# Kernel tuning notes

Hardware: AMD Instinct MI355X
Metric: run time of the kernel (lower is better)

The kernel has to match this reference:

```python
import jax, jax.numpy as jnp
import numpy as np

B, D, H, K = 32768, 64, 512, 8
P = 3 * K - 1            # widths(K) + heights(K) + interior derivatives(K-1)
BOUND = 4.0
MIN_BIN = 1e-3           # min bin width/height fraction
MIN_DERIV = 1e-3


def setup_inputs() -> dict:
    key = jax.random.key(0)
    k0, k1, k2, k3 = jax.random.split(key, 4)
    x = jax.random.normal(k0, (B, D), jnp.float32) * 2.0
    W1 = jax.random.normal(k1, (H, D), jnp.float32) / np.sqrt(D)
    b1 = jnp.zeros((H,), jnp.float32)
    W2 = jax.random.normal(k2, (D * P, H), jnp.float32) / np.sqrt(H)
    b2 = jax.random.normal(k3, (D * P,), jnp.float32) * 0.01
    m_in = np.arange(1, D + 1)                      # input degrees 1..D
    m_hid = (np.arange(H) % (D - 1)) + 1            # hidden degrees 1..D-1
    M1 = jnp.asarray((m_hid[:, None] >= m_in[None, :]).astype(np.float32))   # [H, D]
    m_out = (np.arange(D * P) // P) + 1             # output degree = dim index + 1
    M2 = jnp.asarray((m_out[:, None] > m_hid[None, :]).astype(np.float32))   # [D*P, H]
    return {"x": x, "W1": W1, "b1": b1, "W2": W2, "b2": b2, "M1": M1, "M2": M2}


def _rqs(x, w_un, h_un, d_un):
    """Monotonic rational-quadratic spline (elementwise over [B, D]).
    w_un, h_un: [B, D, K] unnormalized widths/heights; d_un: [B, D, K-1].
    Returns (y [B, D], logabsdet [B, D])."""
    f32 = x.dtype
    w = jax.nn.softmax(w_un, axis=-1)
    hh = jax.nn.softmax(h_un, axis=-1)
    w = MIN_BIN + (1.0 - MIN_BIN * K) * w
    hh = MIN_BIN + (1.0 - MIN_BIN * K) * hh
    edge_lo = jnp.full(w.shape[:-1] + (1,), -BOUND, f32)
    edge_hi = jnp.full(w.shape[:-1] + (1,), BOUND, f32)
    # knot positions [B, D, K+1] with exact endpoints at +-BOUND
    xk = jnp.concatenate([edge_lo, -BOUND + 2.0 * BOUND * jnp.cumsum(w, -1)[..., :-1], edge_hi], -1)
    yk = jnp.concatenate([edge_lo, -BOUND + 2.0 * BOUND * jnp.cumsum(hh, -1)[..., :-1], edge_hi], -1)
    widths = xk[..., 1:] - xk[..., :-1]
    heights = yk[..., 1:] - yk[..., :-1]
    ones = jnp.ones(w.shape[:-1] + (1,), f32)
    # boundary derivatives fixed to 1 (identity outside the box)
    d = jnp.concatenate([ones, MIN_DERIV + jax.nn.softplus(d_un), ones], -1)  # [B, D, K+1]

    inside = (x >= -BOUND) & (x <= BOUND)
    xc = jnp.clip(x, -BOUND, BOUND)
    # bucketize: index of containing bin
    idx = jnp.clip(jnp.sum((xc[..., None] >= xk).astype(jnp.int32), -1) - 1, 0, K - 1)

    def g(a, off=0):
        return jnp.take_along_axis(a, idx[..., None] + off, axis=-1)[..., 0]

    x_k, y_k = g(xk), g(yk)
    w_k, h_k = g(widths), g(heights)
    d_k, d_k1 = g(d), g(d, 1)
    s = h_k / w_k
    theta = (xc - x_k) / w_k
    t1m = theta * (1.0 - theta)
    num = h_k * (s * theta * theta + d_k * t1m)
    den = s + (d_k1 + d_k - 2.0 * s) * t1m
    y_in = y_k + num / den
    dnum = s * s * (d_k1 * theta * theta + 2.0 * s * t1m + d_k * (1.0 - theta) ** 2)
    ld_in = jnp.log(dnum) - 2.0 * jnp.log(den)
    y = jnp.where(inside, y_in, x)
    ld = jnp.where(inside, ld_in, 0.0)
    return y, ld


def _forward(x, W1, b1, W2, b2, M1, M2):
    hmid = jax.nn.relu(x @ (W1 * M1).T + b1)          # [B, H]
    params = (hmid @ (W2 * M2).T + b2).reshape(x.shape[0], D, P)
    w_un = params[..., :K]
    h_un = params[..., K:2 * K]
    d_un = params[..., 2 * K:]
    z, ld = _rqs(x, w_un, h_un, d_un)
    return z, jnp.sum(ld, axis=-1)                    # logDet per example


def reference(x, W1, b1, W2, b2, M1, M2):
    return _forward(x, W1, b1, W2, b2, M1, M2)
```

## Files before the change

kernel.cpp:

```cpp
#include <hip/hip_runtime.h>
#include <math.h>

#define NB    32768
#define DDIM  64
#define HDIM  512
#define PDIM  23
#define KBINS 8
#define BM    32
#define NCOLS (DDIM * PDIM)
#define CHUNK 368
#define PSTRIDE 372
#define NTILES 92

#define RQ_BOUND  4.0f
#define RQ_MINBIN 0.001f
#define RQ_MINDER 0.001f

typedef __attribute__((ext_vector_type(8))) _Float16 half8;
typedef __attribute__((ext_vector_type(4))) float f32x4;
typedef unsigned short ushort_t;

__global__ __launch_bounds__(256) void prep_frag(const float* __restrict__ W1,
                                                 const float* __restrict__ W2,
                                                 _Float16* __restrict__ W1g,
                                                 _Float16* __restrict__ W2g) {
    const int gid = blockIdx.x * 256 + threadIdx.x;
    const int NW1 = 32 * 2 * 64;
    if (gid < NW1) {
        const int lane = gid & 63;
        const int tk   = gid >> 6;
        const int kt   = tk & 1, ht = tk >> 1;
        const int h = ht * 16 + (lane & 15);
        const int k = kt * 32 + (lane >> 4) * 8;
        const float* src = W1 + h * DDIM + k;
        const int hm63 = h % 63;
        half8 v;
        #pragma unroll
        for (int e = 0; e < 8; ++e)
            v[e] = (_Float16)(((k + e) <= hm63) ? src[e] : 0.0f);
        *(half8*)(W1g + (size_t)gid * 8) = v;
    } else {
        const int g2 = gid - NW1;
        if (g2 < NTILES * 16 * 64) {
            const int lane = g2 & 63;
            const int tk   = g2 >> 6;
            const int kt   = tk & 15, T = tk >> 4;
            const int col  = T * 16 + (lane & 15);
            const int k    = kt * 32 + (lane >> 4) * 8;
            const float* src = W2 + (size_t)col * HDIM + k;
            const int d = col / PDIM;
            half8 v;
            #pragma unroll
            for (int e = 0; e < 8; ++e)
                v[e] = (_Float16)((d > ((k + e) % 63)) ? src[e] : 0.0f);
            *(half8*)(W2g + (size_t)g2 * 8) = v;
        }
    }
}

__device__ __forceinline__ float fexp(float v)  { return __expf(v); }
__device__ __forceinline__ float flog(float v)  { return __logf(v); }
__device__ __forceinline__ float fdiv(float a, float b) { return __fdividef(a, b); }

__device__ __forceinline__ void rqs_eval(const float* prm, float xorig,
                                         float& yo, float& ldo) {
    const float xc = fminf(fmaxf(xorig, -RQ_BOUND), RQ_BOUND);
    const bool inside = (xorig >= -RQ_BOUND) && (xorig <= RQ_BOUND);

    float xk[KBINS + 1], yk[KBINS + 1], dd[KBINS + 1];
    {
        float m = prm[0];
        #pragma unroll
        for (int i = 1; i < KBINS; ++i) m = fmaxf(m, prm[i]);
        float e[KBINS]; float s = 0.0f;
        #pragma unroll
        for (int i = 0; i < KBINS; ++i) { e[i] = fexp(prm[i] - m); s += e[i]; }
        const float inv = fdiv(1.0f, s);
        float c = 0.0f;
        xk[0] = -RQ_BOUND;
        #pragma unroll
        for (int i = 0; i < KBINS; ++i) {
            float w = RQ_MINBIN + (1.0f - RQ_MINBIN * KBINS) * (e[i] * inv);
            c += w;
            xk[i + 1] = -RQ_BOUND + 2.0f * RQ_BOUND * c;
        }
        xk[KBINS] = RQ_BOUND;
    }
    {
        float m = prm[8];
        #pragma unroll
        for (int i = 1; i < KBINS; ++i) m = fmaxf(m, prm[8 + i]);
        float e[KBINS]; float s = 0.0f;
        #pragma unroll
        for (int i = 0; i < KBINS; ++i) { e[i] = fexp(prm[8 + i] - m); s += e[i]; }
        const float inv = fdiv(1.0f, s);
        float c = 0.0f;
        yk[0] = -RQ_BOUND;
        #pragma unroll
        for (int i = 0; i < KBINS; ++i) {
            float h = RQ_MINBIN + (1.0f - RQ_MINBIN * KBINS) * (e[i] * inv);
            c += h;
            yk[i + 1] = -RQ_BOUND + 2.0f * RQ_BOUND * c;
        }
        yk[KBINS] = RQ_BOUND;
    }
    dd[0] = 1.0f;
    #pragma unroll
    for (int i = 0; i < KBINS - 1; ++i) {
        const float v = prm[16 + i];
        const float e = fexp(-fabsf(v));
        dd[i + 1] = RQ_MINDER + flog(1.0f + e) + fmaxf(v, 0.0f);
    }
    dd[KBINS] = 1.0f;

    int idx = 0;
    #pragma unroll
    for (int i = 1; i < KBINS; ++i) idx += (xc >= xk[i]) ? 1 : 0;

    float x_k = xk[0], x_k1 = xk[1];
    float y_k = yk[0], y_k1 = yk[1];
    float d_k = dd[0], d_k1 = dd[1];
    #pragma unroll
    for (int i = 1; i < KBINS; ++i) {
        const bool mm = (idx == i);
        x_k  = mm ? xk[i]     : x_k;
        x_k1 = mm ? xk[i + 1] : x_k1;
        y_k  = mm ? yk[i]     : y_k;
        y_k1 = mm ? yk[i + 1] : y_k1;
        d_k  = mm ? dd[i]     : d_k;
        d_k1 = mm ? dd[i + 1] : d_k1;
    }

    const float w_k = x_k1 - x_k;
    const float h_k = y_k1 - y_k;
    const float rw  = fdiv(1.0f, w_k);
    const float s   = h_k * rw;
    const float th  = (xc - x_k) * rw;
    const float omt = 1.0f - th;
    const float t1m = th * omt;
    const float num = h_k * (s * th * th + d_k * t1m);
    const float den = s + (d_k1 + d_k - 2.0f * s) * t1m;
    const float yin = y_k + fdiv(num, den);
    const float dnum = s * s * (d_k1 * th * th + 2.0f * s * t1m + d_k * omt * omt);
    const float ldin = flog(dnum) - 2.0f * flog(den);

    yo  = inside ? yin : xorig;
    ldo = inside ? ldin : 0.0f;
}

__global__ __launch_bounds__(512, 4) void fused_flow(
    const float* __restrict__ x,  const float* __restrict__ b1,
    const float* __restrict__ b2, const _Float16* __restrict__ W1g,
    const _Float16* __restrict__ W2g,
    float* __restrict__ z_out, float* __restrict__ ld_out)
{
    __shared__ __align__(16) ushort_t hm[BM * 512];
    __shared__ __align__(16) float pstage[BM * PSTRIDE];

    const int t    = threadIdx.x;
    const int row0 = blockIdx.x * BM;
    const int wv   = t >> 6;
    const int lane = t & 63;
    const int l15  = lane & 15;
    const int lg   = lane >> 4;

    char* hmB = (char*)hm;

    {
        f32x4 acc1[4][2];
        #pragma unroll
        for (int j = 0; j < 4; ++j)
            #pragma unroll
            for (int m = 0; m < 2; ++m) acc1[j][m] = (f32x4){0.f, 0.f, 0.f, 0.f};

        #pragma unroll
        for (int kt = 0; kt < 2; ++kt) {
            half8 a[2];
            #pragma unroll
            for (int m = 0; m < 2; ++m) {
                const float* xr = x + (size_t)(row0 + m * 16 + l15) * DDIM + kt * 32 + lg * 8;
                const float4 xa = *(const float4*)(xr);
                const float4 xb = *(const float4*)(xr + 4);
                a[m][0] = (_Float16)xa.x; a[m][1] = (_Float16)xa.y;
                a[m][2] = (_Float16)xa.z; a[m][3] = (_Float16)xa.w;
                a[m][4] = (_Float16)xb.x; a[m][5] = (_Float16)xb.y;
                a[m][6] = (_Float16)xb.z; a[m][7] = (_Float16)xb.w;
            }
            #pragma unroll
            for (int j = 0; j < 4; ++j) {
                const half8 b = *(const half8*)(W1g + (size_t)(wv * 4 + j) * 1024 + kt * 512 + lane * 8);
                #pragma unroll
                for (int m = 0; m < 2; ++m)
                    acc1[j][m] = __builtin_amdgcn_mfma_f32_16x16x32_f16(a[m], b, acc1[j][m], 0, 0, 0);
            }
        }
        #pragma unroll
        for (int j = 0; j < 4; ++j) {
            const int h = (wv * 4 + j) * 16 + l15;
            const float bias = b1[h];
            #pragma unroll
            for (int m = 0; m < 2; ++m) {
                #pragma unroll
                for (int q = 0; q < 4; ++q) {
                    const int r = m * 16 + lg * 4 + q;
                    const _Float16 hv = (_Float16)fmaxf(acc1[j][m][q] + bias, 0.0f);
                    *(ushort_t*)(hmB + r * 1024 + ((h * 2) ^ ((r & 7) << 4))) =
                        __builtin_bit_cast(ushort_t, hv);
                }
            }
        }
    }
    __syncthreads();

    float ldacc = 0.0f;
    const int srow = t >> 4;
    const int sd   = t & 15;
    const int tbase = wv * 3;

    const _Float16* w2base[3];
    #pragma unroll
    for (int i = 0; i < 3; ++i) {
        const int tile = (tbase + i < 23) ? (tbase + i) : 22;
        w2base[i] = W2g + (size_t)tile * 8192 + lane * 8;
    }

    for (int c = 0; c < 4; ++c) {
        f32x4 acc[3][2];
        #pragma unroll
        for (int i = 0; i < 3; ++i)
            #pragma unroll
            for (int m = 0; m < 2; ++m) acc[i][m] = (f32x4){0.f, 0.f, 0.f, 0.f};

        const size_t coff = (size_t)c * (23 * 8192);

        #pragma unroll 4
        for (int kt = 0; kt < 16; ++kt) {
            half8 ah[2];
            #pragma unroll
            for (int m = 0; m < 2; ++m) {
                const int r  = m * 16 + l15;
                const int kb = (kt * 32 + lg * 8) * 2;
                ah[m] = *(const half8*)(hmB + r * 1024 + (kb ^ ((r & 7) << 4)));
            }
            half8 bfr[3];
            #pragma unroll
            for (int i = 0; i < 3; ++i)
                bfr[i] = *(const half8*)(w2base[i] + coff + kt * 512);
            #pragma unroll
            for (int i = 0; i < 3; ++i)
                #pragma unroll
                for (int m = 0; m < 2; ++m)
                    acc[i][m] = __builtin_amdgcn_mfma_f32_16x16x32_f16(ah[m], bfr[i], acc[i][m], 0, 0, 0);
        }

        __syncthreads();

        #pragma unroll
        for (int i = 0; i < 3; ++i) {
            if (tbase + i < 23) {
                const int lcol = (tbase + i) * 16 + l15;
                #pragma unroll
                for (int m = 0; m < 2; ++m)
                    #pragma unroll
                    for (int q = 0; q < 4; ++q)
                        pstage[(m * 16 + lg * 4 + q) * PSTRIDE + lcol] = acc[i][m][q];
            }
        }
        __syncthreads();

        {
            const int d = c * 16 + sd;
            float prm[PDIM];
            #pragma unroll
            for (int p = 0; p < PDIM; ++p)
                prm[p] = pstage[srow * PSTRIDE + sd * PDIM + p] + b2[d * PDIM + p];
            const float xv = x[(size_t)(row0 + srow) * DDIM + d];
            float yv, lv;
            rqs_eval(prm, xv, yv, lv);
            z_out[(size_t)(row0 + srow) * DDIM + d] = yv;
            ldacc += lv;
        }
    }

    ldacc += __shfl_xor(ldacc, 1, 64);
    ldacc += __shfl_xor(ldacc, 2, 64);
    ldacc += __shfl_xor(ldacc, 4, 64);
    ldacc += __shfl_xor(ldacc, 8, 64);
    if (sd == 0) ld_out[row0 + srow] = ldacc;
}

extern "C" void kernel_launch(void* const* d_in, const int* in_sizes, int n_in,
                              void* d_out, int out_size, void* d_ws, size_t ws_size,
                              hipStream_t stream) {
    (void)in_sizes; (void)n_in; (void)out_size; (void)ws_size;
    const float* x  = (const float*)d_in[0];
    const float* W1 = (const float*)d_in[1];
    const float* b1 = (const float*)d_in[2];
    const float* W2 = (const float*)d_in[3];
    const float* b2 = (const float*)d_in[4];

    _Float16* W1g = (_Float16*)d_ws;
    _Float16* W2g = W1g + HDIM * DDIM;
    float* z  = (float*)d_out;
    float* ld = z + (size_t)NB * DDIM;

    const int n_groups = 32 * 2 * 64 + NTILES * 16 * 64;
    prep_frag<<<(n_groups + 255) / 256, 256, 0, stream>>>(W1, W2, W1g, W2g);
    fused_flow<<<NB / BM, 512, 0, stream>>>(x, b1, b2, W1g, W2g, z, ld);
}
```

Baseline: 93.57 us.

## Prefetch next chunk's W2 fragments and simplify spline math

New measurement: 92.47 us. No clear change (-1.2%).

```diff
diff --git a/kernel.cpp b/kernel.cpp
--- a/kernel.cpp
+++ b/kernel.cpp
@@ -66,51 +66,41 @@
                                          float& yo, float& ldo) {
     const float xc = fminf(fmaxf(xorig, -RQ_BOUND), RQ_BOUND);
     const bool inside = (xorig >= -RQ_BOUND) && (xorig <= RQ_BOUND);
+    const float CNORM = 1.0f - RQ_MINBIN * KBINS;
 
     float xk[KBINS + 1], yk[KBINS + 1], dd[KBINS + 1];
     {
-        float m = prm[0];
-        #pragma unroll
-        for (int i = 1; i < KBINS; ++i) m = fmaxf(m, prm[i]);
         float e[KBINS]; float s = 0.0f;
         #pragma unroll
-        for (int i = 0; i < KBINS; ++i) { e[i] = fexp(prm[i] - m); s += e[i]; }
-        const float inv = fdiv(1.0f, s);
+        for (int i = 0; i < KBINS; ++i) { e[i] = fexp(prm[i]); s += e[i]; }
+        const float cinv = CNORM * fdiv(1.0f, s);
         float c = 0.0f;
         xk[0] = -RQ_BOUND;
         #pragma unroll
         for (int i = 0; i < KBINS; ++i) {
-            float w = RQ_MINBIN + (1.0f - RQ_MINBIN * KBINS) * (e[i] * inv);
-            c += w;
-            xk[i + 1] = -RQ_BOUND + 2.0f * RQ_BOUND * c;
+            c += fmaf(e[i], cinv, RQ_MINBIN);
+            xk[i + 1] = fmaf(c, 2.0f * RQ_BOUND, -RQ_BOUND);
         }
         xk[KBINS] = RQ_BOUND;
     }
     {
-        float m = prm[8];
-        #pragma unroll
-        for (int i = 1; i < KBINS; ++i) m = fmaxf(m, prm[8 + i]);
         float e[KBINS]; float s = 0.0f;
         #pragma unroll
-        for (int i = 0; i < KBINS; ++i) { e[i] = fexp(prm[8 + i] - m); s += e[i]; }
-        const float inv = fdiv(1.0f, s);
+        for (int i = 0; i < KBINS; ++i) { e[i] = fexp(prm[8 + i]); s += e[i]; }
+        const float cinv = CNORM * fdiv(1.0f, s);
         float c = 0.0f;
         yk[0] = -RQ_BOUND;
         #pragma unroll
         for (int i = 0; i < KBINS; ++i) {
-            float h = RQ_MINBIN + (1.0f - RQ_MINBIN * KBINS) * (e[i] * inv);
-            c += h;
-            yk[i + 1] = -RQ_BOUND + 2.0f * RQ_BOUND * c;
+            c += fmaf(e[i], cinv, RQ_MINBIN);
+            yk[i + 1] = fmaf(c, 2.0f * RQ_BOUND, -RQ_BOUND);
         }
         yk[KBINS] = RQ_BOUND;
     }
     dd[0] = 1.0f;
     #pragma unroll
-    for (int i = 0; i < KBINS - 1; ++i) {
-        const float v = prm[16 + i];
-        const float e = fexp(-fabsf(v));
-        dd[i + 1] = RQ_MINDER + flog(1.0f + e) + fmaxf(v, 0.0f);
-    }
+    for (int i = 0; i < KBINS - 1; ++i)
+        dd[i + 1] = RQ_MINDER + flog(1.0f + fexp(prm[16 + i]));
     dd[KBINS] = 1.0f;
 
     int idx = 0;
@@ -142,7 +132,7 @@
     const float den = s + (d_k1 + d_k - 2.0f * s) * t1m;
     const float yin = y_k + fdiv(num, den);
     const float dnum = s * s * (d_k1 * th * th + 2.0f * s * t1m + d_k * omt * omt);
-    const float ldin = flog(dnum) - 2.0f * flog(den);
+    const float ldin = flog(fdiv(dnum, den * den));
 
     yo  = inside ? yin : xorig;
     ldo = inside ? ldin : 0.0f;
@@ -224,6 +214,13 @@
         w2base[i] = W2g + (size_t)tile * 8192 + lane * 8;
     }
 
+    half8 pfb0[3], pfb1[3];
+    #pragma unroll
+    for (int i = 0; i < 3; ++i) {
+        pfb0[i] = *(const half8*)(w2base[i]);
+        pfb1[i] = *(const half8*)(w2base[i] + 512);
+    }
+
     for (int c = 0; c < 4; ++c) {
         f32x4 acc[3][2];
         #pragma unroll
@@ -233,8 +230,8 @@
 
         const size_t coff = (size_t)c * (23 * 8192);
 
-        #pragma unroll 4
-        for (int kt = 0; kt < 16; ++kt) {
+        #pragma unroll
+        for (int kt = 0; kt < 2; ++kt) {
             half8 ah[2];
             #pragma unroll
             for (int m = 0; m < 2; ++m) {
@@ -242,6 +239,24 @@
                 const int kb = (kt * 32 + lg * 8) * 2;
                 ah[m] = *(const half8*)(hmB + r * 1024 + (kb ^ ((r & 7) << 4)));
             }
+            #pragma unroll
+            for (int i = 0; i < 3; ++i) {
+                const half8 bf = (kt == 0) ? pfb0[i] : pfb1[i];
+                #pragma unroll
+                for (int m = 0; m < 2; ++m)
+                    acc[i][m] = __builtin_amdgcn_mfma_f32_16x16x32_f16(ah[m], bf, acc[i][m], 0, 0, 0);
+            }
+        }
+
+        #pragma unroll 2
+        for (int kt = 2; kt < 16; ++kt) {
+            half8 ah[2];
+            #pragma unroll
+            for (int m = 0; m < 2; ++m) {
+                const int r  = m * 16 + l15;
+                const int kb = (kt * 32 + lg * 8) * 2;
+                ah[m] = *(const half8*)(hmB + r * 1024 + (kb ^ ((r & 7) << 4)));
+            }
             half8 bfr[3];
             #pragma unroll
             for (int i = 0; i < 3; ++i)
@@ -267,6 +282,15 @@
             }
         }
         __syncthreads();
+
+        {
+            const size_t ncoff = (size_t)(c < 3 ? c + 1 : 3) * (23 * 8192);
+            #pragma unroll
+            for (int i = 0; i < 3; ++i) {
+                pfb0[i] = *(const half8*)(w2base[i] + ncoff);
+                pfb1[i] = *(const half8*)(w2base[i] + ncoff + 512);
+            }
+        }
 
         {
             const int d = c * 16 + sd;
```

## Warp-specialize GEMM producers and spline consumers with double-buffered param staging

Applied to the files above, without the earlier changes.

After: 95.46 us. 2.0% more time.

```diff
diff --git a/kernel.cpp b/kernel.cpp
--- a/kernel.cpp
+++ b/kernel.cpp
@@ -8,9 +8,11 @@
 #define KBINS 8
 #define BM    32
 #define NCOLS (DDIM * PDIM)
-#define CHUNK 368
-#define PSTRIDE 372
-#define NTILES 92
+#define CH2   184
+#define NCH   8
+#define TPC   12
+#define PSTR2 185
+#define PBUFH (BM * PSTR2)
 
 #define RQ_BOUND  4.0f
 #define RQ_MINBIN 0.001f
@@ -41,11 +43,14 @@
         *(half8*)(W1g + (size_t)gid * 8) = v;
     } else {
         const int g2 = gid - NW1;
-        if (g2 < NTILES * 16 * 64) {
+        if (g2 < 96 * 16 * 64) {
             const int lane = g2 & 63;
             const int tk   = g2 >> 6;
-            const int kt   = tk & 15, T = tk >> 4;
-            const int col  = T * 16 + (lane & 15);
+            const int kt   = tk & 15, tt = tk >> 4;
+            const int c    = tt / TPC;
+            const int i    = tt - c * TPC;
+            const int colbase = c * CH2 + (i < 11 ? i * 16 : 168);
+            const int col  = colbase + (lane & 15);
             const int k    = kt * 32 + (lane >> 4) * 8;
             const float* src = W2 + (size_t)col * HDIM + k;
             const int d = col / PDIM;
@@ -66,51 +71,41 @@
                                          float& yo, float& ldo) {
     const float xc = fminf(fmaxf(xorig, -RQ_BOUND), RQ_BOUND);
     const bool inside = (xorig >= -RQ_BOUND) && (xorig <= RQ_BOUND);
+    const float CNORM = 1.0f - RQ_MINBIN * KBINS;
 
     float xk[KBINS + 1], yk[KBINS + 1], dd[KBINS + 1];
     {
-        float m = prm[0];
-        #pragma unroll
-        for (int i = 1; i < KBINS; ++i) m = fmaxf(m, prm[i]);
         float e[KBINS]; float s = 0.0f;
         #pragma unroll
-        for (int i = 0; i < KBINS; ++i) { e[i] = fexp(prm[i] - m); s += e[i]; }
-        const float inv = fdiv(1.0f, s);
+        for (int i = 0; i < KBINS; ++i) { e[i] = fexp(prm[i]); s += e[i]; }
+        const float cinv = CNORM * fdiv(1.0f, s);
         float c = 0.0f;
         xk[0] = -RQ_BOUND;
         #pragma unroll
         for (int i = 0; i < KBINS; ++i) {
-            float w = RQ_MINBIN + (1.0f - RQ_MINBIN * KBINS) * (e[i] * inv);
-            c += w;
-            xk[i + 1] = -RQ_BOUND + 2.0f * RQ_BOUND * c;
+            c += fmaf(e[i], cinv, RQ_MINBIN);
+            xk[i + 1] = fmaf(c, 2.0f * RQ_BOUND, -RQ_BOUND);
         }
         xk[KBINS] = RQ_BOUND;
     }
     {
-        float m = prm[8];
-        #pragma unroll
-        for (int i = 1; i < KBINS; ++i) m = fmaxf(m, prm[8 + i]);
         float e[KBINS]; float s = 0.0f;
         #pragma unroll
-        for (int i = 0; i < KBINS; ++i) { e[i] = fexp(prm[8 + i] - m); s += e[i]; }
-        const float inv = fdiv(1.0f, s);
+        for (int i = 0; i < KBINS; ++i) { e[i] = fexp(prm[8 + i]); s += e[i]; }
+        const float cinv = CNORM * fdiv(1.0f, s);
         float c = 0.0f;
         yk[0] = -RQ_BOUND;
         #pragma unroll
         for (int i = 0; i < KBINS; ++i) {
-            float h = RQ_MINBIN + (1.0f - RQ_MINBIN * KBINS) * (e[i] * inv);
-            c += h;
-            yk[i + 1] = -RQ_BOUND + 2.0f * RQ_BOUND * c;
+            c += fmaf(e[i], cinv, RQ_MINBIN);
+            yk[i + 1] = fmaf(c, 2.0f * RQ_BOUND, -RQ_BOUND);
         }
         yk[KBINS] = RQ_BOUND;
     }
     dd[0] = 1.0f;
     #pragma unroll
-    for (int i = 0; i < KBINS - 1; ++i) {
-        const float v = prm[16 + i];
-        const float e = fexp(-fabsf(v));
-        dd[i + 1] = RQ_MINDER + flog(1.0f + e) + fmaxf(v, 0.0f);
-    }
+    for (int i = 0; i < KBINS - 1; ++i)
+        dd[i + 1] = RQ_MINDER + flog(1.0f + fexp(prm[16 + i]));
     dd[KBINS] = 1.0f;
 
     int idx = 0;
@@ -142,7 +137,7 @@
     const float den = s + (d_k1 + d_k - 2.0f * s) * t1m;
     const float yin = y_k + fdiv(num, den);
     const float dnum = s * s * (d_k1 * th * th + 2.0f * s * t1m + d_k * omt * omt);
-    const float ldin = flog(dnum) - 2.0f * flog(den);
+    const float ldin = flog(fdiv(dnum, den * den));
 
     yo  = inside ? yin : xorig;
     ldo = inside ? ldin : 0.0f;
@@ -155,7 +150,7 @@
     float* __restrict__ z_out, float* __restrict__ ld_out)
 {
     __shared__ __align__(16) ushort_t hm[BM * 512];
-    __shared__ __align__(16) float pstage[BM * PSTRIDE];
+    __shared__ __align__(16) float pbuf[2 * PBUFH];
 
     const int t    = threadIdx.x;
     const int row0 = blockIdx.x * BM;
@@ -212,27 +207,29 @@
     }
     __syncthreads();
 
+    const bool producer = (wv < 6);
+    const int  tloc = t - 384;
+    const int  srow = tloc & 31;
+    const int  dq   = tloc >> 5;
+
+    const _Float16* w2base[2];
+    #pragma unroll
+    for (int i = 0; i < 2; ++i) {
+        const int j = (2 * wv + i < TPC) ? (2 * wv + i) : (TPC - 1);
+        w2base[i] = W2g + (size_t)j * 8192 + lane * 8;
+    }
+
     float ldacc = 0.0f;
-    const int srow = t >> 4;
-    const int sd   = t & 15;
-    const int tbase = wv * 3;
-
-    const _Float16* w2base[3];
-    #pragma unroll
-    for (int i = 0; i < 3; ++i) {
-        const int tile = (tbase + i < 23) ? (tbase + i) : 22;
-        w2base[i] = W2g + (size_t)tile * 8192 + lane * 8;
-    }
-
-    for (int c = 0; c < 4; ++c) {
-        f32x4 acc[3][2];
-        #pragma unroll
-        for (int i = 0; i < 3; ++i)
+    float z0a, z0b, z1a, z1b, z2a, z2b, z3a, z3b;
+    float z4a, z4b, z5a, z5b, z6a, z6b, z7a, z7b;
+
+    auto PROD = [&](int C) {
+        f32x4 acc[2][2];
+        #pragma unroll
+        for (int i = 0; i < 2; ++i)
             #pragma unroll
             for (int m = 0; m < 2; ++m) acc[i][m] = (f32x4){0.f, 0.f, 0.f, 0.f};
-
-        const size_t coff = (size_t)c * (23 * 8192);
-
+        const size_t coff = (size_t)C * (TPC * 8192);
         #pragma unroll 4
         for (int kt = 0; kt < 16; ++kt) {
             half8 ah[2];
@@ -242,51 +239,87 @@
                 const int kb = (kt * 32 + lg * 8) * 2;
                 ah[m] = *(const half8*)(hmB + r * 1024 + (kb ^ ((r & 7) << 4)));
             }
-            half8 bfr[3];
-            #pragma unroll
-            for (int i = 0; i < 3; ++i)
+            half8 bfr[2];
+            #pragma unroll
+            for (int i = 0; i < 2; ++i)
                 bfr[i] = *(const half8*)(w2base[i] + coff + kt * 512);
             #pragma unroll
-            for (int i = 0; i < 3; ++i)
+            for (int i = 0; i < 2; ++i)
                 #pragma unroll
                 for (int m = 0; m < 2; ++m)
                     acc[i][m] = __builtin_amdgcn_mfma_f32_16x16x32_f16(ah[m], bfr[i], acc[i][m], 0, 0, 0);
         }
-
-        __syncthreads();
-
-        #pragma unroll
-        for (int i = 0; i < 3; ++i) {
-            if (tbase + i < 23) {
-                const int lcol = (tbase + i) * 16 + l15;
+        float* pb = pbuf + (C & 1) * PBUFH;
+        #pragma unroll
+        for (int i = 0; i < 2; ++i) {
+            const int j = 2 * wv + i;
+            const int lcol = (j < 11 ? j * 16 : 168) + l15;
+            if (j < 11 || l15 >= 8) {
+                const float bb = b2[C * CH2 + lcol];
                 #pragma unroll
                 for (int m = 0; m < 2; ++m)
                     #pragma unroll
                     for (int q = 0; q < 4; ++q)
-                        pstage[(m * 16 + lg * 4 + q) * PSTRIDE + lcol] = acc[i][m][q];
-            }
-        }
-        __syncthreads();
-
-        {
-            const int d = c * 16 + sd;
-            float prm[PDIM];
-            #pragma unroll
-            for (int p = 0; p < PDIM; ++p)
-                prm[p] = pstage[srow * PSTRIDE + sd * PDIM + p] + b2[d * PDIM + p];
-            const float xv = x[(size_t)(row0 + srow) * DDIM + d];
-            float yv, lv;
-            rqs_eval(prm, xv, yv, lv);
-            z_out[(size_t)(row0 + srow) * DDIM + d] = yv;
-            ldacc += lv;
-        }
-    }
-
-    ldacc += __shfl_xor(ldacc, 1, 64);
-    ldacc += __shfl_xor(ldacc, 2, 64);
-    ldacc += __shfl_xor(ldacc, 4, 64);
-    ldacc += __shfl_xor(ldacc, 8, 64);
-    if (sd == 0) ld_out[row0 + srow] = ldacc;
+                        pb[(m * 16 + lg * 4 + q) * PSTR2 + lcol] = acc[i][m][q] + bb;
+            }
+        }
+    };
+
+    auto EVAL = [&](int sc, int dloc, float& zdst) {
+        const float* pb = pbuf + (sc & 1) * PBUFH + srow * PSTR2 + dloc * PDIM;
+        float prm[PDIM];
+        #pragma unroll
+        for (int p = 0; p < PDIM; ++p) prm[p] = pb[p];
+        const int d = sc * 8 + dloc;
+        const float xv = x[(size_t)(row0 + srow) * DDIM + d];
+        float yv, lv;
+        rqs_eval(prm, xv, yv, lv);
+        zdst = yv;
+        ldacc += lv;
+    };
+
+    #define STEP(C, ZA, ZB)                                             \
+        __syncthreads();                                                \
+        if (producer) { PROD(C); }                                      \
+        else { EVAL(C - 1, dq, ZA); EVAL(C - 1, dq + 4, ZB); }
+
+    __syncthreads();
+    if (producer) PROD(0);
+    STEP(1, z0a, z0b)
+    STEP(2, z1a, z1b)
+    STEP(3, z2a, z2b)
+    STEP(4, z3a, z3b)
+    STEP(5, z4a, z4b)
+    STEP(6, z5a, z5b)
+    STEP(7, z6a, z6b)
+    __syncthreads();
+    if (!producer) { EVAL(7, dq, z7a); EVAL(7, dq + 4, z7b); }
+    #undef STEP
+
+    if (!producer) {
+        float* zls = pbuf;
+        #define ZSC(SC, ZA, ZB)                         \
+            zls[srow * 65 + SC * 8 + dq]     = ZA;      \
+            zls[srow * 65 + SC * 8 + dq + 4] = ZB;
+        ZSC(0, z0a, z0b) ZSC(1, z1a, z1b) ZSC(2, z2a, z2b) ZSC(3, z3a, z3b)
+        ZSC(4, z4a, z4b) ZSC(5, z5a, z5b) ZSC(6, z6a, z6b) ZSC(7, z7a, z7b)
+        #undef ZSC
+        ldacc += __shfl_xor(ldacc, 32, 64);
+        if (lane < 32) zls[2080 + (wv - 6) * 32 + srow] = ldacc;
+    }
+    __syncthreads();
+    {
+        const int r  = t >> 4;
+        const int d0 = (t & 15) * 4;
+        const float* zls = pbuf;
+        float4 zv;
+        zv.x = zls[r * 65 + d0 + 0];
+        zv.y = zls[r * 65 + d0 + 1];
+        zv.z = zls[r * 65 + d0 + 2];
+        zv.w = zls[r * 65 + d0 + 3];
+        *(float4*)(z_out + (size_t)(row0 + r) * DDIM + d0) = zv;
+    }
+    if (t < BM) ld_out[row0 + t] = pbuf[2080 + t] + pbuf[2112 + t];
 }
 
 extern "C" void kernel_launch(void* const* d_in, const int* in_sizes, int n_in,
@@ -304,7 +337,7 @@
     float* z  = (float*)d_out;
     float* ld = z + (size_t)NB * DDIM;
 
-    const int n_groups = 32 * 2 * 64 + NTILES * 16 * 64;
+    const int n_groups = 32 * 2 * 64 + 96 * 16 * 64;
     prep_frag<<<(n_groups + 255) / 256, 256, 0, stream>>>(W1, W2, W1g, W2g);
     fused_flow<<<NB / BM, 512, 0, stream>>>(x, b1, b2, W1g, W2g, z, ld);
 }
```

## Software-pipeline spline evaluation of previous chunk with MFMA GEMM of next chunk

Applied to the files above, without the earlier changes.

Result: faster. 90.47 us (median of 2 runs) (-3.3%).

```diff
diff --git a/kernel.cpp b/kernel.cpp
--- a/kernel.cpp
+++ b/kernel.cpp
@@ -62,92 +62,6 @@
 __device__ __forceinline__ float flog(float v)  { return __logf(v); }
 __device__ __forceinline__ float fdiv(float a, float b) { return __fdividef(a, b); }
 
-__device__ __forceinline__ void rqs_eval(const float* prm, float xorig,
-                                         float& yo, float& ldo) {
-    const float xc = fminf(fmaxf(xorig, -RQ_BOUND), RQ_BOUND);
-    const bool inside = (xorig >= -RQ_BOUND) && (xorig <= RQ_BOUND);
-
-    float xk[KBINS + 1], yk[KBINS + 1], dd[KBINS + 1];
-    {
-        float m = prm[0];
-        #pragma unroll
-        for (int i = 1; i < KBINS; ++i) m = fmaxf(m, prm[i]);
-        float e[KBINS]; float s = 0.0f;
-        #pragma unroll
-        for (int i = 0; i < KBINS; ++i) { e[i] = fexp(prm[i] - m); s += e[i]; }
-        const float inv = fdiv(1.0f, s);
-        float c = 0.0f;
-        xk[0] = -RQ_BOUND;
-        #pragma unroll
-        for (int i = 0; i < KBINS; ++i) {
-            float w = RQ_MINBIN + (1.0f - RQ_MINBIN * KBINS) * (e[i] * inv);
-            c += w;
-            xk[i + 1] = -RQ_BOUND + 2.0f * RQ_BOUND * c;
-        }
-        xk[KBINS] = RQ_BOUND;
-    }
-    {
-        float m = prm[8];
-        #pragma unroll
-        for (int i = 1; i < KBINS; ++i) m = fmaxf(m, prm[8 + i]);
-        float e[KBINS]; float s = 0.0f;
-        #pragma unroll
-        for (int i = 0; i < KBINS; ++i) { e[i] = fexp(prm[8 + i] - m); s += e[i]; }
-        const float inv = fdiv(1.0f, s);
-        float c = 0.0f;
-        yk[0] = -RQ_BOUND;
-        #pragma unroll
-        for (int i = 0; i < KBINS; ++i) {
-            float h = RQ_MINBIN + (1.0f - RQ_MINBIN * KBINS) * (e[i] * inv);
-            c += h;
-            yk[i + 1] = -RQ_BOUND + 2.0f * RQ_BOUND * c;
-        }
-        yk[KBINS] = RQ_BOUND;
-    }
-    dd[0] = 1.0f;
-    #pragma unroll
-    for (int i = 0; i < KBINS - 1; ++i) {
-        const float v = prm[16 + i];
-        const float e = fexp(-fabsf(v));
-        dd[i + 1] = RQ_MINDER + flog(1.0f + e) + fmaxf(v, 0.0f);
-    }
-    dd[KBINS] = 1.0f;
-
-    int idx = 0;
-    #pragma unroll
-    for (int i = 1; i < KBINS; ++i) idx += (xc >= xk[i]) ? 1 : 0;
-
-    float x_k = xk[0], x_k1 = xk[1];
-    float y_k = yk[0], y_k1 = yk[1];
-    float d_k = dd[0], d_k1 = dd[1];
-    #pragma unroll
-    for (int i = 1; i < KBINS; ++i) {
-        const bool mm = (idx == i);
-        x_k  = mm ? xk[i]     : x_k;
-        x_k1 = mm ? xk[i + 1] : x_k1;
-        y_k  = mm ? yk[i]     : y_k;
-        y_k1 = mm ? yk[i + 1] : y_k1;
-        d_k  = mm ? dd[i]     : d_k;
-        d_k1 = mm ? dd[i + 1] : d_k1;
-    }
-
-    const float w_k = x_k1 - x_k;
-    const float h_k = y_k1 - y_k;
-    const float rw  = fdiv(1.0f, w_k);
-    const float s   = h_k * rw;
-    const float th  = (xc - x_k) * rw;
-    const float omt = 1.0f - th;
-    const float t1m = th * omt;
-    const float num = h_k * (s * th * th + d_k * t1m);
-    const float den = s + (d_k1 + d_k - 2.0f * s) * t1m;
-    const float yin = y_k + fdiv(num, den);
-    const float dnum = s * s * (d_k1 * th * th + 2.0f * s * t1m + d_k * omt * omt);
-    const float ldin = flog(dnum) - 2.0f * flog(den);
-
-    yo  = inside ? yin : xorig;
-    ldo = inside ? ldin : 0.0f;
-}
-
 __global__ __launch_bounds__(512, 4) void fused_flow(
     const float* __restrict__ x,  const float* __restrict__ b1,
     const float* __restrict__ b2, const _Float16* __restrict__ W1g,
@@ -216,6 +130,7 @@
     const int srow = t >> 4;
     const int sd   = t & 15;
     const int tbase = wv * 3;
+    const float CNORM = 1.0f - RQ_MINBIN * KBINS;
 
     const _Float16* w2base[3];
     #pragma unroll
@@ -224,63 +139,174 @@
         w2base[i] = W2g + (size_t)tile * 8192 + lane * 8;
     }
 
-    for (int c = 0; c < 4; ++c) {
-        f32x4 acc[3][2];
-        #pragma unroll
-        for (int i = 0; i < 3; ++i)
-            #pragma unroll
-            for (int m = 0; m < 2; ++m) acc[i][m] = (f32x4){0.f, 0.f, 0.f, 0.f};
-
-        const size_t coff = (size_t)c * (23 * 8192);
-
-        #pragma unroll 4
-        for (int kt = 0; kt < 16; ++kt) {
-            half8 ah[2];
-            #pragma unroll
-            for (int m = 0; m < 2; ++m) {
-                const int r  = m * 16 + l15;
-                const int kb = (kt * 32 + lg * 8) * 2;
-                ah[m] = *(const half8*)(hmB + r * 1024 + (kb ^ ((r & 7) << 4)));
-            }
-            half8 bfr[3];
-            #pragma unroll
-            for (int i = 0; i < 3; ++i)
-                bfr[i] = *(const half8*)(w2base[i] + coff + kt * 512);
-            #pragma unroll
-            for (int i = 0; i < 3; ++i)
-                #pragma unroll
-                for (int m = 0; m < 2; ++m)
-                    acc[i][m] = __builtin_amdgcn_mfma_f32_16x16x32_f16(ah[m], bfr[i], acc[i][m], 0, 0, 0);
-        }
-
-        __syncthreads();
-
-        #pragma unroll
-        for (int i = 0; i < 3; ++i) {
-            if (tbase + i < 23) {
-                const int lcol = (tbase + i) * 16 + l15;
-                #pragma unroll
-                for (int m = 0; m < 2; ++m)
-                    #pragma unroll
-                    for (int q = 0; q < 4; ++q)
-                        pstage[(m * 16 + lg * 4 + q) * PSTRIDE + lcol] = acc[i][m][q];
-            }
-        }
-        __syncthreads();
-
-        {
-            const int d = c * 16 + sd;
-            float prm[PDIM];
-            #pragma unroll
-            for (int p = 0; p < PDIM; ++p)
-                prm[p] = pstage[srow * PSTRIDE + sd * PDIM + p] + b2[d * PDIM + p];
-            const float xv = x[(size_t)(row0 + srow) * DDIM + d];
-            float yv, lv;
-            rqs_eval(prm, xv, yv, lv);
-            z_out[(size_t)(row0 + srow) * DDIM + d] = yv;
-            ldacc += lv;
-        }
-    }
+    f32x4 acc[3][2];
+    float xk[KBINS + 1], yk[KBINS + 1], dv[KBINS + 1];
+
+#define ZERO_ACC                                                            \
+    _Pragma("unroll")                                                       \
+    for (int i = 0; i < 3; ++i)                                             \
+        _Pragma("unroll")                                                   \
+        for (int m = 0; m < 2; ++m) acc[i][m] = (f32x4){0.f, 0.f, 0.f, 0.f};
+
+#define KTG(CN, K0)                                                         \
+    {                                                                       \
+        const size_t coff = (size_t)(CN) * (23 * 8192);                     \
+        _Pragma("unroll")                                                   \
+        for (int kt = (K0); kt < (K0) + 4; ++kt) {                          \
+            half8 ah[2];                                                    \
+            _Pragma("unroll")                                               \
+            for (int m = 0; m < 2; ++m) {                                   \
+                const int r  = m * 16 + l15;                                \
+                const int kb = (kt * 32 + lg * 8) * 2;                      \
+                ah[m] = *(const half8*)(hmB + r * 1024 + (kb ^ ((r & 7) << 4))); \
+            }                                                               \
+            half8 bfr[3];                                                   \
+            _Pragma("unroll")                                               \
+            for (int i = 0; i < 3; ++i)                                     \
+                bfr[i] = *(const half8*)(w2base[i] + coff + kt * 512);      \
+            _Pragma("unroll")                                               \
+            for (int i = 0; i < 3; ++i)                                     \
+                _Pragma("unroll")                                           \
+                for (int m = 0; m < 2; ++m)                                 \
+                    acc[i][m] = __builtin_amdgcn_mfma_f32_16x16x32_f16(ah[m], bfr[i], acc[i][m], 0, 0, 0); \
+        }                                                                   \
+    }
+
+#define STAGE(CN)                                                           \
+    _Pragma("unroll")                                                       \
+    for (int i = 0; i < 3; ++i) {                                           \
+        if (tbase + i < 23) {                                               \
+            const int lcol = (tbase + i) * 16 + l15;                        \
+            _Pragma("unroll")                                               \
+            for (int m = 0; m < 2; ++m)                                     \
+                _Pragma("unroll")                                           \
+                for (int q = 0; q < 4; ++q)                                 \
+                    pstage[(m * 16 + lg * 4 + q) * PSTRIDE + lcol] = acc[i][m][q]; \
+        }                                                                   \
+    }
+
+#define SPL_A(CS)                                                           \
+    {                                                                       \
+        const float* pp = &pstage[srow * PSTRIDE + sd * PDIM];              \
+        const float* bp = b2 + (size_t)((CS) * 16 + sd) * PDIM;             \
+        float e[8]; float s = 0.0f;                                         \
+        _Pragma("unroll")                                                   \
+        for (int i = 0; i < 8; ++i) { e[i] = fexp(pp[i] + bp[i]); s += e[i]; } \
+        const float cinv = CNORM * fdiv(1.0f, s);                           \
+        float cum = 0.0f;                                                   \
+        xk[0] = -RQ_BOUND;                                                  \
+        _Pragma("unroll")                                                   \
+        for (int i = 0; i < 8; ++i) {                                       \
+            cum += fmaf(e[i], cinv, RQ_MINBIN);                             \
+            xk[i + 1] = fmaf(cum, 2.0f * RQ_BOUND, -RQ_BOUND);              \
+        }                                                                   \
+        xk[KBINS] = RQ_BOUND;                                               \
+    }
+
+#define SPL_B(CS)                                                           \
+    {                                                                       \
+        const float* pp = &pstage[srow * PSTRIDE + sd * PDIM];              \
+        const float* bp = b2 + (size_t)((CS) * 16 + sd) * PDIM;             \
+        float e[8]; float s = 0.0f;                                         \
+        _Pragma("unroll")                                                   \
+        for (int i = 0; i < 8; ++i) { e[i] = fexp(pp[8 + i] + bp[8 + i]); s += e[i]; } \
+        const float cinv = CNORM * fdiv(1.0f, s);                           \
+        float cum = 0.0f;                                                   \
+        yk[0] = -RQ_BOUND;                                                  \
+        _Pragma("unroll")                                                   \
+        for (int i = 0; i < 8; ++i) {                                       \
+            cum += fmaf(e[i], cinv, RQ_MINBIN);                             \
+            yk[i + 1] = fmaf(cum, 2.0f * RQ_BOUND, -RQ_BOUND);              \
+        }                                                                   \
+        yk[KBINS] = RQ_BOUND;                                               \
+    }
+
+#define SPL_C(CS)                                                           \
+    {                                                                       \
+        const float* pp = &pstage[srow * PSTRIDE + sd * PDIM];              \
+        const float* bp = b2 + (size_t)((CS) * 16 + sd) * PDIM;             \
+        dv[0] = 1.0f;                                                       \
+        _Pragma("unroll")                                                   \
+        for (int i = 0; i < 7; ++i)                                         \
+            dv[i + 1] = RQ_MINDER + flog(1.0f + fexp(pp[16 + i] + bp[16 + i])); \
+        dv[KBINS] = 1.0f;                                                   \
+    }
+
+#define SPL_D(CS)                                                           \
+    {                                                                       \
+        const int dcol = (CS) * 16 + sd;                                    \
+        const float xorig = x[(size_t)(row0 + srow) * DDIM + dcol];         \
+        const float xc = fminf(fmaxf(xorig, -RQ_BOUND), RQ_BOUND);          \
+        const bool inside = (xorig >= -RQ_BOUND) && (xorig <= RQ_BOUND);    \
+        int idx = 0;                                                        \
+        _Pragma("unroll")                                                   \
+        for (int i = 1; i < KBINS; ++i) idx += (xc >= xk[i]) ? 1 : 0;       \
+        float x_k = xk[0], x_k1 = xk[1];                                    \
+        float y_k = yk[0], y_k1 = yk[1];                                    \
+        float d_k = dv[0], d_k1 = dv[1];                                    \
+        _Pragma("unroll")                                                   \
+        for (int i = 1; i < KBINS; ++i) {                                   \
+            const bool mm = (idx == i);                                     \
+            x_k  = mm ? xk[i]     : x_k;                                    \
+            x_k1 = mm ? xk[i + 1] : x_k1;                                   \
+            y_k  = mm ? yk[i]     : y_k;                                    \
+            y_k1 = mm ? yk[i + 1] : y_k1;                                   \
+            d_k  = mm ? dv[i]     : d_k;                                    \
+            d_k1 = mm ? dv[i + 1] : d_k1;                                   \
+        }                                                                   \
+        const float w_k = x_k1 - x_k;                                       \
+        const float h_k = y_k1 - y_k;                                       \
+        const float rw  = fdiv(1.0f, w_k);                                  \
+        const float sv  = h_k * rw;                                         \
+        const float th  = (xc - x_k) * rw;                                  \
+        const float omt = 1.0f - th;                                        \
+        const float t1m = th * omt;                                         \
+        const float num = h_k * (sv * th * th + d_k * t1m);                 \
+        const float den = sv + (d_k1 + d_k - 2.0f * sv) * t1m;              \
+        const float yin = y_k + fdiv(num, den);                             \
+        const float dnum = sv * sv * (d_k1 * th * th + 2.0f * sv * t1m + d_k * omt * omt); \
+        const float ldin = flog(fdiv(dnum, den * den));                     \
+        z_out[(size_t)(row0 + srow) * DDIM + dcol] = inside ? yin : xorig;  \
+        ldacc += inside ? ldin : 0.0f;                                      \
+    }
+
+#define MERGED(CN, CS)                                                      \
+    ZERO_ACC                                                                \
+    KTG(CN, 0)  SPL_A(CS)                                                   \
+    KTG(CN, 4)  SPL_B(CS)                                                   \
+    KTG(CN, 8)  SPL_C(CS)                                                   \
+    KTG(CN, 12) SPL_D(CS)
+
+    ZERO_ACC
+    KTG(0, 0) KTG(0, 4) KTG(0, 8) KTG(0, 12)
+    STAGE(0)
+    __syncthreads();
+
+    MERGED(1, 0)
+    __syncthreads();
+    STAGE(1)
+    __syncthreads();
+
+    MERGED(2, 1)
+    __syncthreads();
+    STAGE(2)
+    __syncthreads();
+
+    MERGED(3, 2)
+    __syncthreads();
+    STAGE(3)
+    __syncthreads();
+
+    SPL_A(3) SPL_B(3) SPL_C(3) SPL_D(3)
+
+#undef MERGED
+#undef SPL_D
+#undef SPL_C
+#undef SPL_B
+#undef SPL_A
+#undef STAGE
+#undef KTG
+#undef ZERO_ACC
 
     ldacc += __shfl_xor(ldacc, 1, 64);
     ldacc += __shfl_xor(ldacc, 2, 64);
```
